# Performance work log

Hardware: AMD Instinct MI355X
Metric: run time of the kernel (lower is better)

Reference implementation:

```python
import jax, jax.numpy as jnp
import numpy as np

DIM = 1024
NUM_HEADS = 16
HEAD_DIM = DIM // NUM_HEADS
SCALE = HEAD_DIM ** -0.5


def setup_inputs() -> dict:
    key = jax.random.key(0)
    ks = jax.random.split(key, 5)
    B, N, C = 2, 2048, DIM
    x = jax.random.normal(ks[0], (B, N, C), dtype=jnp.float32)
    s = 1.0 / np.sqrt(C)
    W_qkv = jax.random.normal(ks[1], (C, 3 * C), dtype=jnp.float32) * s
    b_qkv = jax.random.normal(ks[2], (3 * C,), dtype=jnp.float32) * 0.01
    W_proj = jax.random.normal(ks[3], (C, C), dtype=jnp.float32) * s
    b_proj = jax.random.normal(ks[4], (C,), dtype=jnp.float32) * 0.01
    return {"x": x, "W_qkv": W_qkv, "b_qkv": b_qkv, "W_proj": W_proj, "b_proj": b_proj}


def reference(x, W_qkv, b_qkv, W_proj, b_proj):
    B, N, C = x.shape
    qkv = x @ W_qkv + b_qkv                      # [B, N, 3C]
    qkv = qkv.reshape(B, N, 3, NUM_HEADS, HEAD_DIM)
    qkv = jnp.transpose(qkv, (2, 0, 3, 1, 4))    # [3, B, H, N, hd]
    # Faithful to source quirk: q = k = v = qkv[2]
    v = qkv[2]
    q = v
    k = v
    attn = jnp.einsum('bhnd,bhmd->bhnm', q, k) * SCALE
    attn = jax.nn.softmax(attn, axis=-1)
    out = jnp.einsum('bhnm,bhmd->bhnd', attn, v)  # [B, H, N, hd]
    out = jnp.transpose(out, (0, 2, 1, 3)).reshape(B, N, C)
    return out @ W_proj + b_proj
```

## Files before the change

### kernel.cpp

```cpp
#include <hip/hip_runtime.h>

typedef __bf16    bf16x4 __attribute__((ext_vector_type(4)));
typedef __bf16    bf16x8 __attribute__((ext_vector_type(8)));
typedef _Float16  f16x2  __attribute__((ext_vector_type(2)));
typedef _Float16  f16x4  __attribute__((ext_vector_type(4)));
typedef _Float16  f16x8  __attribute__((ext_vector_type(8)));
typedef float     f32x4  __attribute__((ext_vector_type(4)));

#define MFMA16x16x32 __builtin_amdgcn_mfma_f32_16x16x32_bf16
#define MFMA16x16x16F __builtin_amdgcn_mfma_f32_16x16x16f16

__device__ __forceinline__ void gload_lds16(const void* g, void* l) {
  __builtin_amdgcn_global_load_lds((const __attribute__((address_space(1))) void*)g,
                                   (__attribute__((address_space(3))) void*)l, 16, 0, 0);
}

__device__ __forceinline__ f16x2 pkrtz(float a, float b) {
  return __builtin_bit_cast(f16x2, __builtin_amdgcn_cvt_pkrtz(a, b));
}

__global__ __launch_bounds__(256) void cvt_f32_bf16(const float* __restrict__ src,
                                                    __bf16* __restrict__ dst, int n4) {
  int i = blockIdx.x * 256 + threadIdx.x;
  if (i >= n4) return;
  const float4 f = ((const float4*)src)[i];
  bf16x4 o;
  o.x = (__bf16)f.x; o.y = (__bf16)f.y; o.z = (__bf16)f.z; o.w = (__bf16)f.w;
  ((bf16x4*)dst)[i] = o;
}

__global__ __launch_bounds__(256) void prep_transpose(const float* __restrict__ Wqkv,
                                                      const float* __restrict__ Wproj,
                                                      __bf16* __restrict__ WvT,
                                                      __bf16* __restrict__ WpT) {
  __shared__ float tile[64][65];
  const float* src; __bf16* dst; int ld, c0;
  if (blockIdx.z == 0) { src = Wqkv; dst = WvT; ld = 3072; c0 = 2048; }
  else                 { src = Wproj; dst = WpT; ld = 1024; c0 = 0; }
  const int k0 = blockIdx.x * 64, n0 = blockIdx.y * 64;
  const int t = threadIdx.x;
#pragma unroll
  for (int i = 0; i < 4; i++) {
    int idx = t + i * 256; int r = idx >> 4, g = idx & 15;
    float4 v = *(const float4*)&src[(size_t)(k0 + r) * ld + c0 + n0 + g * 4];
    tile[r][g * 4 + 0] = v.x; tile[r][g * 4 + 1] = v.y;
    tile[r][g * 4 + 2] = v.z; tile[r][g * 4 + 3] = v.w;
  }
  __syncthreads();
#pragma unroll
  for (int i = 0; i < 4; i++) {
    int idx = t + i * 256; int n = idx >> 4, g = idx & 15;
    bf16x4 o;
    o.x = (__bf16)tile[g * 4 + 0][n]; o.y = (__bf16)tile[g * 4 + 1][n];
    o.z = (__bf16)tile[g * 4 + 2][n]; o.w = (__bf16)tile[g * 4 + 3][n];
    *(bf16x4*)&dst[(size_t)(n0 + n) * 1024 + k0 + g * 4] = o;
  }
}

__global__ __launch_bounds__(256) void build_vt(const __bf16* __restrict__ V,
                                                _Float16* __restrict__ Vt) {
  __shared__ _Float16 tl[64][72];
  const int bh = blockIdx.y, b = bh >> 4, h = bh & 15;
  const int n0 = blockIdx.x * 64;
  const int t = threadIdx.x;
#pragma unroll
  for (int i = 0; i < 2; i++) {
    int idx = t + i * 256; int r = idx >> 3, g = idx & 7;
    bf16x8 v = *(const bf16x8*)&V[(size_t)(b * 2048 + n0 + r) * 1024 + h * 64 + g * 8];
    f16x8 c;
#pragma unroll
    for (int j = 0; j < 8; j++) c[j] = (_Float16)(float)v[j];
    *(f16x8*)&tl[r][g * 8] = c;
  }
  __syncthreads();
#pragma unroll
  for (int i = 0; i < 2; i++) {
    int idx = t + i * 256; int d = idx >> 3, g = idx & 7;
    f16x8 o;
#pragma unroll
    for (int j = 0; j < 8; j++) o[j] = tl[g * 8 + j][d];
    *(f16x8*)&Vt[((size_t)bh * 64 + d) * 2048 + n0 + g * 8] = o;
  }
}

template <bool BF16OUT>
__global__ __launch_bounds__(256, 4) void gemm_bt(const __bf16* __restrict__ A,
                                                  const __bf16* __restrict__ Bt,
                                                  const float* __restrict__ bias,
                                                  void* __restrict__ outp) {
  constexpr int K = 1024, Nn = 1024;
  __shared__ __bf16 lds[2 * 4096];
  const int t = threadIdx.x, w = t >> 6, l = t & 63, lr = l & 15, quad = l >> 4;
  const int m0 = blockIdx.x * 64, n0 = blockIdx.y * 64;
  const int rm = t >> 2, kg = t & 3;

  const __bf16* pA = A  + (size_t)(m0 + rm) * K + kg * 8;
  const __bf16* pB = Bt + (size_t)(n0 + rm) * K + kg * 8;

  f32x4 acc[4] = {};

  gload_lds16(pA, (char*)lds + t * 16);
  gload_lds16(pB, (char*)lds + 4096 + t * 16);
  for (int it = 0; it < 32; ++it) {
    __syncthreads();
    if (it + 1 < 32) {
      pA += 32; pB += 32;
      char* buf = (char*)lds + ((it + 1) & 1) * 8192;
      gload_lds16(pA, buf + t * 16);
      gload_lds16(pB, buf + 4096 + t * 16);
    }
    const __bf16* Al = lds + (it & 1) * 4096;
    const __bf16* Bl = Al + 2048;
    bf16x8 af = *(const bf16x8*)&Al[(w * 16 + lr) * 32 + quad * 8];
#pragma unroll
    for (int nc = 0; nc < 4; nc++) {
      bf16x8 bv = *(const bf16x8*)&Bl[(nc * 16 + lr) * 32 + quad * 8];
      acc[nc] = MFMA16x16x32(af, bv, acc[nc], 0, 0, 0);
    }
  }
#pragma unroll
  for (int nc = 0; nc < 4; nc++)
#pragma unroll
    for (int r = 0; r < 4; r++) {
      int grow = m0 + w * 16 + quad * 4 + r;
      int gcol = n0 + nc * 16 + lr;
      float v = acc[nc][r] + bias[gcol];
      if (BF16OUT) ((__bf16*)outp)[(size_t)grow * Nn + gcol] = (__bf16)v;
      else         ((float*)outp)[(size_t)grow * Nn + gcol] = v;
    }
}

__global__ __launch_bounds__(512, 4) void attn_kernel(const __bf16* __restrict__ V,
                                                      const _Float16* __restrict__ Vt,
                                                      __bf16* __restrict__ O) {
  __shared__ char lds[65536];
  const int t = threadIdx.x, w = t >> 6, l = t & 63, lr = l & 15, quad = l >> 4;
  const int bh = blockIdx.x, b = bh >> 4, h = bh & 15;
  const int qb = blockIdx.y * 128 + (w & 3) * 16;
  const int part = w >> 2;

  const __bf16* Vbh = V + (size_t)b * 2048 * 1024 + h * 64;
  const _Float16* Vtbh = Vt + (size_t)bh * 64 * 2048;

  bf16x8 qf[2][2];
#pragma unroll
  for (int sub = 0; sub < 2; sub++)
#pragma unroll
    for (int ks = 0; ks < 2; ks++)
      qf[sub][ks] = *(const bf16x8*)(Vbh + (size_t)(qb + sub * 64 + lr) * 1024 + ks * 32 + quad * 8);

  const int kva = t >> 3, ua = (t & 7) ^ (kva & 7);
  const __bf16* pK0 = Vbh + (size_t)kva * 1024 + ua * 8;
  const __bf16* pK1 = pK0 + (size_t)64 * 1024;
  const int kb_ = t >> 7, d_ = (t >> 1) & 63, qh = (t & 1) ^ ((d_ >> 2) & 1);
  const _Float16* pV0 = Vtbh + (size_t)d_ * 2048 + kb_ * 16 + qh * 8;
  const _Float16* pV1 = pV0 + 64;

  const int koff0 = lr * 128 + ((quad ^ (lr & 7)) * 16);
  const int koff1 = lr * 128 + (((4 + quad) ^ (lr & 7)) * 16);
  const int xq = (quad >> 1) ^ ((lr >> 2) & 1);
  const int voff = lr * 32 + xq * 16 + (quad & 1) * 8;

  f32x4 o[2][4] = {};
  f32x4 l5[2] = {};
  f16x4 ones; ones[0] = ones[1] = ones[2] = ones[3] = (_Float16)1.0f;
  const float Cc = 0.18033688011112042f;
  const float C8 = 11.541560327111707f;

  {
    char* base = lds;
    gload_lds16(pK0, base + t * 16);
    gload_lds16(pV0, base + 8192 + t * 16);
    gload_lds16(pK1, base + 16384 + t * 16);
    gload_lds16(pV1, base + 24576 + t * 16);
  }
  for (int it = 0; it < 16; ++it) {
    __syncthreads();
    if (it + 1 < 16) {
      pK0 += 131072; pK1 += 131072; pV0 += 128; pV1 += 128;
      char* base = lds + ((it + 1) & 1) * 32768;
      gload_lds16(pK0, base + t * 16);
      gload_lds16(pV0, base + 8192 + t * 16);
      gload_lds16(pK1, base + 16384 + t * 16);
      gload_lds16(pV1, base + 24576 + t * 16);
    }
    const char* Kb = lds + (it & 1) * 32768 + part * 16384;
    const char* Vb = Kb + 8192;

    f32x4 s[2][4] = {};
#pragma unroll
    for (int ks = 0; ks < 2; ks++) {
      const int ko = ks ? koff1 : koff0;
#pragma unroll
      for (int rb = 0; rb < 4; rb++) {
        bf16x8 kf = *(const bf16x8*)(Kb + ko + rb * 2048);
        s[0][rb] = MFMA16x16x32(kf, qf[0][ks], s[0][rb], 0, 0, 0);
        s[1][rb] = MFMA16x16x32(kf, qf[1][ks], s[1][rb], 0, 0, 0);
      }
    }

    f16x4 pf[2][4];
#pragma unroll
    for (int sub = 0; sub < 2; sub++)
#pragma unroll
      for (int rb = 0; rb < 4; rb++) {
        float p0 = __builtin_amdgcn_exp2f(s[sub][rb][0] * Cc - C8);
        float p1 = __builtin_amdgcn_exp2f(s[sub][rb][1] * Cc - C8);
        float p2 = __builtin_amdgcn_exp2f(s[sub][rb][2] * Cc - C8);
        float p3 = __builtin_amdgcn_exp2f(s[sub][rb][3] * Cc - C8);
        f16x2 lo = pkrtz(p0, p1);
        f16x2 hi = pkrtz(p2, p3);
        pf[sub][rb][0] = lo[0]; pf[sub][rb][1] = lo[1];
        pf[sub][rb][2] = hi[0]; pf[sub][rb][3] = hi[1];
      }

#pragma unroll
    for (int kb = 0; kb < 4; kb++) {
#pragma unroll
      for (int db = 0; db < 4; db++) {
        f16x4 vf = *(const f16x4*)(Vb + voff + db * 512 + kb * 2048);
        o[0][db] = MFMA16x16x16F(pf[0][kb], vf, o[0][db], 0, 0, 0);
        o[1][db] = MFMA16x16x16F(pf[1][kb], vf, o[1][db], 0, 0, 0);
      }
      l5[0] = MFMA16x16x16F(pf[0][kb], ones, l5[0], 0, 0, 0);
      l5[1] = MFMA16x16x16F(pf[1][kb], ones, l5[1], 0, 0, 0);
    }
  }

  __syncthreads();
  float* xch = (float*)lds;
  if (w >= 4) {
    float* dsto = xch + (w - 4) * 2048;
#pragma unroll
    for (int sub = 0; sub < 2; sub++)
#pragma unroll
      for (int db = 0; db < 4; db++)
        *(f32x4*)&dsto[(sub * 4 + db) * 256 + l * 4] = o[sub][db];
    float* dstl = xch + 8192 + (w - 4) * 512;
    *(f32x4*)&dstl[l * 4] = l5[0];
    *(f32x4*)&dstl[256 + l * 4] = l5[1];
  }
  __syncthreads();
  if (w < 4) {
    const float* srco = xch + w * 2048;
    const float* srcl = xch + 8192 + w * 512;
#pragma unroll
    for (int sub = 0; sub < 2; sub++) {
#pragma unroll
      for (int db = 0; db < 4; db++)
        o[sub][db] += *(const f32x4*)&srco[(sub * 4 + db) * 256 + l * 4];
      l5[sub] += *(const f32x4*)&srcl[sub * 256 + l * 4];
    }
#pragma unroll
    for (int sub = 0; sub < 2; sub++)
#pragma unroll
      for (int r = 0; r < 4; r++) {
        float lv = 1.0f / l5[sub][r];
        int token = b * 2048 + qb + sub * 64 + quad * 4 + r;
#pragma unroll
        for (int db = 0; db < 4; db++)
          O[(size_t)token * 1024 + h * 64 + db * 16 + lr] = (__bf16)(o[sub][db][r] * lv);
      }
  }
}

extern "C" void kernel_launch(void* const* d_in, const int* in_sizes, int n_in,
                              void* d_out, int out_size, void* d_ws, size_t ws_size,
                              hipStream_t stream) {
  (void)in_sizes; (void)n_in; (void)out_size; (void)ws_size;
  const float* x     = (const float*)d_in[0];
  const float* Wqkv  = (const float*)d_in[1];
  const float* bqkv  = (const float*)d_in[2];
  const float* Wproj = (const float*)d_in[3];
  const float* bproj = (const float*)d_in[4];

  char* ws = (char*)d_ws;
  __bf16*    xb  = (__bf16*)(ws);
  __bf16*    V   = (__bf16*)(ws + (size_t)8  * 1048576);
  _Float16*  Vt  = (_Float16*)(ws + (size_t)16 * 1048576);
  __bf16*    Ob  = (__bf16*)(ws + (size_t)24 * 1048576);
  __bf16*    WvT = (__bf16*)(ws + (size_t)32 * 1048576);
  __bf16*    WpT = (__bf16*)(ws + (size_t)34 * 1048576);

  cvt_f32_bf16<<<4096, 256, 0, stream>>>(x, xb, 1048576);
  prep_transpose<<<dim3(16, 16, 2), 256, 0, stream>>>(Wqkv, Wproj, WvT, WpT);
  gemm_bt<true><<<dim3(64, 16), 256, 0, stream>>>(xb, WvT, bqkv + 2048, V);
  build_vt<<<dim3(32, 32), 256, 0, stream>>>(V, Vt);
  attn_kernel<<<dim3(32, 16), 512, 0, stream>>>(V, Vt, Ob);
  gemm_bt<false><<<dim3(64, 16), 256, 0, stream>>>(Ob, WpT, bproj, d_out);
}
```

Before: 166.7 us.

## Fuse x conversion and V transpose into the V projection GEMM

Removes the separate f32-to-bf16 conversion kernel and the build_vt transpose kernel. The V GEMM now loads fp32 x tiles directly into LDS with an XOR swizzle and converts them to bf16 in registers. Its epilogue writes both the bf16 V and the transposed fp16 Vt. This saves two launches and their global round trips, at the cost of larger fp32 A tiles in LDS, per-iteration conversion work, and scattered f16x4 transposed stores.

```diff
diff --git a/kernel.cpp b/kernel.cpp
--- a/kernel.cpp
+++ b/kernel.cpp
@@ -17,16 +17,6 @@
 
 __device__ __forceinline__ f16x2 pkrtz(float a, float b) {
   return __builtin_bit_cast(f16x2, __builtin_amdgcn_cvt_pkrtz(a, b));
-}
-
-__global__ __launch_bounds__(256) void cvt_f32_bf16(const float* __restrict__ src,
-                                                    __bf16* __restrict__ dst, int n4) {
-  int i = blockIdx.x * 256 + threadIdx.x;
-  if (i >= n4) return;
-  const float4 f = ((const float4*)src)[i];
-  bf16x4 o;
-  o.x = (__bf16)f.x; o.y = (__bf16)f.y; o.z = (__bf16)f.z; o.w = (__bf16)f.w;
-  ((bf16x4*)dst)[i] = o;
 }
 
 __global__ __launch_bounds__(256) void prep_transpose(const float* __restrict__ Wqkv,
@@ -57,37 +47,79 @@
   }
 }
 
-__global__ __launch_bounds__(256) void build_vt(const __bf16* __restrict__ V,
-                                                _Float16* __restrict__ Vt) {
-  __shared__ _Float16 tl[64][72];
-  const int bh = blockIdx.y, b = bh >> 4, h = bh & 15;
-  const int n0 = blockIdx.x * 64;
-  const int t = threadIdx.x;
-#pragma unroll
-  for (int i = 0; i < 2; i++) {
-    int idx = t + i * 256; int r = idx >> 3, g = idx & 7;
-    bf16x8 v = *(const bf16x8*)&V[(size_t)(b * 2048 + n0 + r) * 1024 + h * 64 + g * 8];
-    f16x8 c;
-#pragma unroll
-    for (int j = 0; j < 8; j++) c[j] = (_Float16)(float)v[j];
-    *(f16x8*)&tl[r][g * 8] = c;
-  }
-  __syncthreads();
-#pragma unroll
-  for (int i = 0; i < 2; i++) {
-    int idx = t + i * 256; int d = idx >> 3, g = idx & 7;
-    f16x8 o;
-#pragma unroll
-    for (int j = 0; j < 8; j++) o[j] = tl[g * 8 + j][d];
-    *(f16x8*)&Vt[((size_t)bh * 64 + d) * 2048 + n0 + g * 8] = o;
-  }
-}
-
-template <bool BF16OUT>
-__global__ __launch_bounds__(256, 4) void gemm_bt(const __bf16* __restrict__ A,
-                                                  const __bf16* __restrict__ Bt,
-                                                  const float* __restrict__ bias,
-                                                  void* __restrict__ outp) {
+__global__ __launch_bounds__(256, 4) void gemm_v(const float* __restrict__ x,
+                                                 const __bf16* __restrict__ WvT,
+                                                 const float* __restrict__ bias,
+                                                 __bf16* __restrict__ V,
+                                                 _Float16* __restrict__ Vt) {
+  constexpr int K = 1024;
+  __shared__ char lds[2 * 12288];
+  const int t = threadIdx.x, w = t >> 6, l = t & 63, lr = l & 15, quad = l >> 4;
+  const int m0 = blockIdx.x * 64, n0 = blockIdx.y * 64;
+
+  const int rmA = t >> 3;
+  const int kgAs = (t & 7) ^ (rmA & 7);
+  const float* pA0 = x + (size_t)(m0 + rmA) * K + kgAs * 4;
+  const float* pA1 = pA0 + (size_t)32 * K;
+  const int rnB = t >> 2, kgB = t & 3;
+  const __bf16* pB = WvT + (size_t)(n0 + rnB) * K + kgB * 8;
+
+  f32x4 acc[4] = {};
+  {
+    char* buf = (char*)lds;
+    gload_lds16(pA0, buf + t * 16);
+    gload_lds16(pA1, buf + (t + 256) * 16);
+    gload_lds16(pB, buf + 8192 + t * 16);
+  }
+  const int rr = w * 16 + lr;
+  const int ga0 = rr * 8 + ((2 * quad) ^ (rr & 7));
+  const int ga1 = rr * 8 + ((2 * quad + 1) ^ (rr & 7));
+  for (int it = 0; it < 32; ++it) {
+    __syncthreads();
+    if (it + 1 < 32) {
+      pA0 += 32; pA1 += 32; pB += 32;
+      char* buf = (char*)lds + ((it + 1) & 1) * 12288;
+      gload_lds16(pA0, buf + t * 16);
+      gload_lds16(pA1, buf + (t + 256) * 16);
+      gload_lds16(pB, buf + 8192 + t * 16);
+    }
+    const char* Abuf = (char*)lds + (it & 1) * 12288;
+    const char* Bbuf = Abuf + 8192;
+    f32x4 a0 = *(const f32x4*)(Abuf + ga0 * 16);
+    f32x4 a1 = *(const f32x4*)(Abuf + ga1 * 16);
+    bf16x8 af;
+    af[0] = (__bf16)a0[0]; af[1] = (__bf16)a0[1]; af[2] = (__bf16)a0[2]; af[3] = (__bf16)a0[3];
+    af[4] = (__bf16)a1[0]; af[5] = (__bf16)a1[1]; af[6] = (__bf16)a1[2]; af[7] = (__bf16)a1[3];
+#pragma unroll
+    for (int nc = 0; nc < 4; nc++) {
+      bf16x8 bv = *(const bf16x8*)(Bbuf + (nc * 16 + lr) * 64 + quad * 16);
+      acc[nc] = MFMA16x16x32(af, bv, acc[nc], 0, 0, 0);
+    }
+  }
+  const int b_ = blockIdx.x >> 5, by = blockIdx.y;
+  const int ntok0 = (m0 & 2047) + w * 16 + quad * 4;
+#pragma unroll
+  for (int nc = 0; nc < 4; nc++) {
+    int gcol = n0 + nc * 16 + lr;
+    float bb = bias[gcol];
+    float v0 = acc[nc][0] + bb, v1 = acc[nc][1] + bb;
+    float v2 = acc[nc][2] + bb, v3 = acc[nc][3] + bb;
+#pragma unroll
+    for (int r = 0; r < 4; r++) {
+      int grow = m0 + w * 16 + quad * 4 + r;
+      float vv = (r == 0) ? v0 : (r == 1) ? v1 : (r == 2) ? v2 : v3;
+      V[(size_t)grow * 1024 + gcol] = (__bf16)vv;
+    }
+    f16x2 lo = pkrtz(v0, v1), hi = pkrtz(v2, v3);
+    f16x4 pv; pv[0] = lo[0]; pv[1] = lo[1]; pv[2] = hi[0]; pv[3] = hi[1];
+    *(f16x4*)&Vt[((size_t)(b_ * 16 + by) * 64 + nc * 16 + lr) * 2048 + ntok0] = pv;
+  }
+}
+
+__global__ __launch_bounds__(256, 4) void gemm_proj(const __bf16* __restrict__ A,
+                                                    const __bf16* __restrict__ Bt,
+                                                    const float* __restrict__ bias,
+                                                    float* __restrict__ outp) {
   constexpr int K = 1024, Nn = 1024;
   __shared__ __bf16 lds[2 * 4096];
   const int t = threadIdx.x, w = t >> 6, l = t & 63, lr = l & 15, quad = l >> 4;
@@ -98,7 +130,6 @@
   const __bf16* pB = Bt + (size_t)(n0 + rm) * K + kg * 8;
 
   f32x4 acc[4] = {};
-
   gload_lds16(pA, (char*)lds + t * 16);
   gload_lds16(pB, (char*)lds + 4096 + t * 16);
   for (int it = 0; it < 32; ++it) {
@@ -124,9 +155,7 @@
     for (int r = 0; r < 4; r++) {
       int grow = m0 + w * 16 + quad * 4 + r;
       int gcol = n0 + nc * 16 + lr;
-      float v = acc[nc][r] + bias[gcol];
-      if (BF16OUT) ((__bf16*)outp)[(size_t)grow * Nn + gcol] = (__bf16)v;
-      else         ((float*)outp)[(size_t)grow * Nn + gcol] = v;
+      outp[(size_t)grow * Nn + gcol] = acc[nc][r] + bias[gcol];
     }
 }
 
@@ -275,17 +304,14 @@
   const float* bproj = (const float*)d_in[4];
 
   char* ws = (char*)d_ws;
-  __bf16*    xb  = (__bf16*)(ws);
-  __bf16*    V   = (__bf16*)(ws + (size_t)8  * 1048576);
-  _Float16*  Vt  = (_Float16*)(ws + (size_t)16 * 1048576);
-  __bf16*    Ob  = (__bf16*)(ws + (size_t)24 * 1048576);
-  __bf16*    WvT = (__bf16*)(ws + (size_t)32 * 1048576);
-  __bf16*    WpT = (__bf16*)(ws + (size_t)34 * 1048576);
-
-  cvt_f32_bf16<<<4096, 256, 0, stream>>>(x, xb, 1048576);
+  __bf16*    V   = (__bf16*)(ws);
+  _Float16*  Vt  = (_Float16*)(ws + (size_t)8  * 1048576);
+  __bf16*    Ob  = (__bf16*)(ws + (size_t)16 * 1048576);
+  __bf16*    WvT = (__bf16*)(ws + (size_t)24 * 1048576);
+  __bf16*    WpT = (__bf16*)(ws + (size_t)26 * 1048576);
+
   prep_transpose<<<dim3(16, 16, 2), 256, 0, stream>>>(Wqkv, Wproj, WvT, WpT);
-  gemm_bt<true><<<dim3(64, 16), 256, 0, stream>>>(xb, WvT, bqkv + 2048, V);
-  build_vt<<<dim3(32, 32), 256, 0, stream>>>(V, Vt);
+  gemm_v<<<dim3(64, 16), 256, 0, stream>>>(x, WvT, bqkv + 2048, V, Vt);
   attn_kernel<<<dim3(32, 16), 512, 0, stream>>>(V, Vt, Ob);
-  gemm_bt<false><<<dim3(64, 16), 256, 0, stream>>>(Ob, WpT, bproj, d_out);
-}
+  gemm_proj<<<dim3(64, 16), 256, 0, stream>>>(Ob, WpT, bproj, (float*)d_out);
+}
```

Result: no change. 165.1 us (-0.9%).
